# Kernel tuning notes

Measured on AMD Instinct MI355X. Metric: run time of the kernel, lower is better.

The kernel has to match this reference:

```python
import jax, jax.numpy as jnp
import numpy as np

N, D, H, O, E, K = 16384, 512, 512, 64, 8, 2


def _layernorm(x, g, b, eps=1e-5):
    mu = jnp.mean(x, axis=-1, keepdims=True)
    var = jnp.var(x, axis=-1, keepdims=True)
    return (x - mu) * jax.lax.rsqrt(var + eps) * g + b


def _gelu(x):
    return jax.nn.gelu(x, approximate=False)  # torch nn.GELU default (erf)


def setup_inputs() -> dict:
    key = jax.random.key(0)
    ks = jax.random.split(key, 20)
    s = 0.02
    return {
        "x": jax.random.normal(ks[0], (N, D), jnp.float32),
        # gate: Linear(D,H) -> LN(H) -> GELU -> Linear(H,E)
        "g_w1": jax.random.normal(ks[1], (D, H), jnp.float32) * s,
        "g_b1": jnp.zeros((H,), jnp.float32),
        "g_ln_g": jnp.ones((H,), jnp.float32),
        "g_ln_b": jnp.zeros((H,), jnp.float32),
        "g_w2": jax.random.normal(ks[2], (H, E), jnp.float32) * s,
        "g_b2": jnp.zeros((E,), jnp.float32),
        # experts (stacked over E): Linear(D,H)+LN+GELU, Linear(H,H)+LN+GELU, Linear(H,O)
        "e_w1": jax.random.normal(ks[3], (E, D, H), jnp.float32) * s,
        "e_b1": jnp.zeros((E, H), jnp.float32),
        "e_ln1_g": jnp.ones((E, H), jnp.float32),
        "e_ln1_b": jnp.zeros((E, H), jnp.float32),
        "e_w2": jax.random.normal(ks[4], (E, H, H), jnp.float32) * s,
        "e_b2": jnp.zeros((E, H), jnp.float32),
        "e_ln2_g": jnp.ones((E, H), jnp.float32),
        "e_ln2_b": jnp.zeros((E, H), jnp.float32),
        "e_w3": jax.random.normal(ks[5], (E, H, O), jnp.float32) * s,
        "e_b3": jnp.zeros((E, O), jnp.float32),
        # output projection Linear(O,O)
        "p_w": jax.random.normal(ks[6], (O, O), jnp.float32) * s,
        "p_b": jnp.zeros((O,), jnp.float32),
    }


def reference(x, g_w1, g_b1, g_ln_g, g_ln_b, g_w2, g_b2,
              e_w1, e_b1, e_ln1_g, e_ln1_b, e_w2, e_b2, e_ln2_g, e_ln2_b,
              e_w3, e_b3, p_w, p_b):
    n = x.shape[0]
    # --- gate ---
    gh = _gelu(_layernorm(x @ g_w1 + g_b1, g_ln_g, g_ln_b))
    gate_logits = gh @ g_w2 + g_b2                      # [N, E]
    gate_weights = jax.nn.softmax(gate_logits, axis=-1)
    top_k_weights, top_k_indices = jax.lax.top_k(gate_weights, K)
    top_k_weights = top_k_weights / jnp.sum(top_k_weights, axis=-1, keepdims=True)
    # dense per-token expert weights [N, E] (sum of top-k weights routed to each expert)
    w_dense = jnp.zeros((n, e_w1.shape[0]), x.dtype).at[
        jnp.arange(n)[:, None], top_k_indices].add(top_k_weights)
    # --- all experts on all tokens (faithful to dense loop) ---
    h1 = _gelu(_layernorm(jnp.einsum('nd,edh->enh', x, e_w1) + e_b1[:, None, :],
                          e_ln1_g[:, None, :], e_ln1_b[:, None, :]))
    h2 = _gelu(_layernorm(jnp.einsum('enh,ehk->enk', h1, e_w2) + e_b2[:, None, :],
                          e_ln2_g[:, None, :], e_ln2_b[:, None, :]))
    expert_out = jnp.einsum('enh,eho->eno', h2, e_w3) + e_b3[:, None, :]  # [E, N, O]
    combined = jnp.einsum('ne,eno->no', w_dense, expert_out)              # [N, O]
    output = combined @ p_w + p_b
    expert_usage = jnp.mean(gate_weights, axis=0)
    return (output, gate_weights, top_k_indices, top_k_weights, expert_usage)
```

## Files before the change

kernel.cpp:

```cpp
#include <hip/hip_runtime.h>
#include <hip/hip_bf16.h>

#define N_TOK 16384
#define MAX_SLOTS 34080
#define MAX_BLOCKS 216

typedef __attribute__((ext_vector_type(8))) short bf16x8;
typedef __attribute__((ext_vector_type(4))) float f32x4;
typedef unsigned short u16;

__device__ __forceinline__ u16 f2bf(float f) {
  __hip_bfloat16 h = __float2bfloat16(f);
  union { __hip_bfloat16 b; u16 u; } c; c.b = h; return c.u;
}
__device__ __forceinline__ float bfbits2f(u16 u) {
  return __uint_as_float(((unsigned)u) << 16);
}
__device__ __forceinline__ float gelu_erf(float x) {
  return 0.5f * x * (1.0f + erff(x * 0.70710678118654752f));
}
__device__ __forceinline__ float gelu_fast(float x) {
  float u = x * (0.79788456f + 0.035677408f * x * x);
  float ex;
  asm("v_exp_f32 %0, %1" : "=v"(ex) : "v"(-2.8853901f * u));
  float den = 1.0f + ex;
  float r;
  asm("v_rcp_f32 %0, %1" : "=v"(r) : "v"(den));
  return x * r;
}
__device__ __forceinline__ void gload16(const u16* g, char* lds) {
  __builtin_amdgcn_global_load_lds(
      (const __attribute__((address_space(1))) void*)g,
      (__attribute__((address_space(3))) void*)lds, 16, 0, 0);
}

__global__ __launch_bounds__(256) void prep_x(const float* __restrict__ x,
                                              u16* __restrict__ xbf,
                                              u16* __restrict__ xlo) {
  size_t i = (size_t)blockIdx.x * 256 + threadIdx.x;
  float4 v = ((const float4*)x)[i];
  float a[4] = {v.x, v.y, v.z, v.w};
  union { u16 us[4]; unsigned long long ll; } hb, lb;
#pragma unroll
  for (int j = 0; j < 4; ++j) {
    u16 hu = f2bf(a[j]);
    hb.us[j] = hu;
    lb.us[j] = f2bf(a[j] - bfbits2f(hu));
  }
  *(unsigned long long*)(xbf + i * 4) = hb.ll;
  *(unsigned long long*)(xlo + i * 4) = lb.ll;
}

template <int C>
__global__ __launch_bounds__(256) void pack_w(const float* __restrict__ src,
                                              u16* __restrict__ dst, int R) {
  __shared__ float tl[64][65];
  const int e = blockIdx.z;
  const int k0 = blockIdx.x * 64, n0 = blockIdx.y * 64;
  const float* s = src + (size_t)e * R * C;
  const int tr = threadIdx.x >> 2;
  const int tc4 = (threadIdx.x & 3) * 16;
#pragma unroll
  for (int j = 0; j < 4; ++j) {
    float4 v = *(const float4*)(s + (size_t)(k0 + tr) * C + n0 + tc4 + j * 4);
    tl[tr][tc4 + j * 4 + 0] = v.x;
    tl[tr][tc4 + j * 4 + 1] = v.y;
    tl[tr][tc4 + j * 4 + 2] = v.z;
    tl[tr][tc4 + j * 4 + 3] = v.w;
  }
  __syncthreads();
  const int nl = threadIdx.x >> 2;
  const int kl = (threadIdx.x & 3) * 16;
  const int n = n0 + nl;
  const int sx = (n >> 1) & 3;
  const int t = (k0 + kl) >> 5;
  const int q0 = ((k0 + kl) & 31) >> 3;
#pragma unroll
  for (int c = 0; c < 2; ++c) {
    int q = q0 + c;
    int p = q ^ sx;
    union { u16 us[8]; unsigned long long ll[2]; } o;
#pragma unroll
    for (int j = 0; j < 8; ++j) o.us[j] = f2bf(tl[kl + c * 8 + j][nl]);
    u16* d = dst + (((size_t)e * (R / 32) + t) * C + n) * 32 + p * 8;
    ((unsigned long long*)d)[0] = o.ll[0];
    ((unsigned long long*)d)[1] = o.ll[1];
  }
}

__global__ __launch_bounds__(256) void prep_wcat(const float* __restrict__ gw1,
                                                 u16* __restrict__ wp) {
  int idx = blockIdx.x * 256 + threadIdx.x;
  int p = idx & 3;
  int n = (idx >> 2) & 511;
  int t = idx >> 11;
  int q = p ^ ((n >> 1) & 3);
  int k0 = t * 32 + q * 8;
  union { u16 us[8]; unsigned long long ll[2]; } o;
#pragma unroll
  for (int j = 0; j < 8; ++j) {
    int k = k0 + j;
    u16 v;
    if (k < 512) {
      v = f2bf(gw1[k * 512 + n]);
    } else if (k < 1024) {
      float w = gw1[(k - 512) * 512 + n];
      v = f2bf(w - bfbits2f(f2bf(w)));
    } else {
      v = f2bf(gw1[(k - 1024) * 512 + n]);
    }
    o.us[j] = v;
  }
  unsigned long long* d = (unsigned long long*)(wp + (size_t)idx * 8);
  d[0] = o.ll[0];
  d[1] = o.ll[1];
}

__global__ __launch_bounds__(256) void prep_w2t(const float* __restrict__ gw2,
                                                float* __restrict__ w2t) {
  int i = blockIdx.x * 256 + threadIdx.x;
  int e = i >> 9, k = i & 511;
  w2t[i] = gw2[k * 8 + e];
}

template <int FM, int ROUTED, int GATHER, int LNOUT, int FAST>
__global__ __launch_bounds__(512, 2) void gemm_core(
    const u16* __restrict__ A, const u16* __restrict__ A2,
    const u16* __restrict__ Wp, long w_estride, int klen, long osplit,
    const float* __restrict__ bias, int b_estride,
    const float* __restrict__ lng, const float* __restrict__ lnb,
    u16* __restrict__ outb, float* __restrict__ outf,
    const int* __restrict__ slot_token, const int* __restrict__ blk_e,
    const int* __restrict__ blk_tok0) {
  constexpr int BM = FM * 32;
  constexpr int AG = FM * 2;
  constexpr int ABYTES = BM * 64;
  constexpr int BUF = ABYTES + 32768;
  constexpr int NL = AG + 32;
  constexpr int L = (NL + 7) / 8;
  constexpr int TSU = 16384;
  extern __shared__ char smem[];

  const int tid = threadIdx.x;
  const int lane = tid & 63;
  const int wv = tid >> 6;
  const int wm = (wv & 1) * (FM * 16);
  const int wn = (wv >> 1) * 128;
  const int l15 = lane & 15;
  const int lk = lane >> 4;
  const int swzk16 = (lk ^ ((l15 >> 1) & 3)) << 4;

  int e, row0, kt0, kbase;
  if (ROUTED) {
    e = blk_e[blockIdx.x];
    if (e < 0) return;
    row0 = blk_tok0[blockIdx.x];
    kt0 = 0; kbase = 0;
  } else {
    e = 0;
    row0 = blockIdx.x * BM;
    kbase = blockIdx.y * klen;
    kt0 = kbase >> 5;
  }
  const u16* We = Wp + (size_t)e * w_estride;

  const int lrq = lane >> 2;
  const int cse = (((lane & 3) ^ ((lane >> 3) & 3)) << 3);
  size_t off[L];
  int ldsoff[L], typ[L];
#pragma unroll
  for (int i = 0; i < L; ++i) {
    int id = wv + 8 * i;
    if (id >= NL) { typ[i] = 2; off[i] = 0; ldsoff[i] = 0; continue; }
    if (id < AG) {
      int lr = id * 16 + lrq;
      long grow = GATHER ? (long)slot_token[row0 + lr] : (long)(row0 + lr);
      off[i] = (size_t)grow * 512 + cse;
      ldsoff[i] = id * 1024 + lane * 16;
      typ[i] = 0;
    } else {
      int bg = id - AG;
      off[i] = (size_t)bg * 512 + lane * 8;
      ldsoff[i] = ABYTES + bg * 1024 + lane * 16;
      typ[i] = 1;
    }
  }

  auto STAGE = [&](int t, char* b) {
    const int kg = kbase + t * 32;
    const u16* Aseg = A;
    int kc = kg;
    if (A2) {
      if (kg >= 1024) { Aseg = A2; kc = kg - 1024; }
      else if (kg >= 512) kc = kg - 512;
    }
    const u16* Bt = We + (size_t)(kt0 + t) * TSU;
#pragma unroll
    for (int i = 0; i < L; ++i) {
      if (typ[i] == 0)      gload16(Aseg + off[i] + kc, b + ldsoff[i]);
      else if (typ[i] == 1) gload16(Bt + off[i], b + ldsoff[i]);
    }
  };

  f32x4 acc[FM][8];
#pragma unroll
  for (int i = 0; i < FM; ++i)
#pragma unroll
    for (int j = 0; j < 8; ++j) acc[i][j] = (f32x4){0.f, 0.f, 0.f, 0.f};

  const int nt = klen / 32;
  char* buf0 = smem;
  char* buf1 = smem + BUF;

  STAGE(0, buf0);
  __syncthreads();
  for (int t = 0; t < nt; ++t) {
    char* cur = (t & 1) ? buf1 : buf0;
    char* nxt = (t & 1) ? buf0 : buf1;
    if (t + 1 < nt) STAGE(t + 1, nxt);
    char* cB = cur + ABYTES;
    bf16x8 af[FM];
#pragma unroll
    for (int fm = 0; fm < FM; ++fm)
      af[fm] = *(const bf16x8*)(cur + (wm + fm * 16 + l15) * 64 + swzk16);
#pragma unroll
    for (int fn = 0; fn < 8; ++fn) {
      bf16x8 bv = *(const bf16x8*)(cB + (wn + fn * 16 + l15) * 64 + swzk16);
#pragma unroll
      for (int fm = 0; fm < FM; ++fm)
        acc[fm][fn] = __builtin_amdgcn_mfma_f32_16x16x32_bf16(
            af[fm], bv, acc[fm][fn], 0, 0, 0);
    }
    __syncthreads();
  }

  if constexpr (LNOUT) {
    const float* be = bias + (size_t)e * b_estride;
    const float* ge = lng + (size_t)e * b_estride;
    const float* bbe = lnb + (size_t)e * b_estride;
    float bias_v[8], g_v[8], b_v[8];
#pragma unroll
    for (int fn = 0; fn < 8; ++fn) {
      int col = wn + fn * 16 + l15;
      bias_v[fn] = be[col]; g_v[fn] = ge[col]; b_v[fn] = bbe[col];
    }
#pragma unroll
    for (int fm = 0; fm < FM; ++fm)
#pragma unroll
      for (int fn = 0; fn < 8; ++fn)
#pragma unroll
        for (int r = 0; r < 4; ++r) acc[fm][fn][r] += bias_v[fn];

    float* redS1 = (float*)smem;
    float* redS2 = redS1 + 4 * BM;
    const int g = wv >> 1;
#pragma unroll
    for (int fm = 0; fm < FM; ++fm)
#pragma unroll
      for (int r = 0; r < 4; ++r) {
        float a1 = 0.f, a2 = 0.f;
#pragma unroll
        for (int fn = 0; fn < 8; ++fn) {
          float v = acc[fm][fn][r];
          a1 += v; a2 += v * v;
        }
#pragma unroll
        for (int m = 1; m < 16; m <<= 1) {
          a1 += __shfl_xor(a1, m, 64);
          a2 += __shfl_xor(a2, m, 64);
        }
        if (l15 == 0) {
          int row = wm + fm * 16 + lk * 4 + r;
          redS1[g * BM + row] = a1;
          redS2[g * BM + row] = a2;
        }
      }
    __syncthreads();
#pragma unroll
    for (int fm = 0; fm < FM; ++fm)
#pragma unroll
      for (int r = 0; r < 4; ++r) {
        int row = wm + fm * 16 + lk * 4 + r;
        float S1 = 0.f, S2 = 0.f;
#pragma unroll
        for (int q = 0; q < 4; ++q) {
          S1 += redS1[q * BM + row];
          S2 += redS2[q * BM + row];
        }
        float mu = S1 * (1.0f / 512.0f);
        float var = S2 * (1.0f / 512.0f) - mu * mu;
        float rs = rsqrtf(var + 1e-5f);
        size_t rowg = (size_t)(row0 + row);
#pragma unroll
        for (int fn = 0; fn < 8; ++fn) {
          int col = wn + fn * 16 + l15;
          float v = (acc[fm][fn][r] - mu) * rs * g_v[fn] + b_v[fn];
          v = FAST ? gelu_fast(v) : gelu_erf(v);
          outb[rowg * 512 + col] = f2bf(v);
        }
      }
  } else {
    float* dst = outf + (size_t)blockIdx.y * osplit;
#pragma unroll
    for (int fm = 0; fm < FM; ++fm)
#pragma unroll
      for (int r = 0; r < 4; ++r) {
        size_t rowg = (size_t)(row0 + wm + fm * 16 + lk * 4 + r);
#pragma unroll
        for (int fn = 0; fn < 8; ++fn)
          dst[rowg * 512 + wn + fn * 16 + l15] = acc[fm][fn][r];
      }
  }
}

__global__ __launch_bounds__(256) void gate2_topk(
    const float* __restrict__ gh0, const float* __restrict__ gh1,
    const float* __restrict__ b1, const float* __restrict__ lng,
    const float* __restrict__ lnb, const float* __restrict__ w2t,
    const float* __restrict__ b2, float* __restrict__ gwout,
    float* __restrict__ idxout, float* __restrict__ tkwout) {
  const int lane = threadIdx.x & 63;
  const int wv = threadIdx.x >> 6;
  const int t = blockIdx.x * 4 + wv;
  const int c0 = lane * 8;
  float v[8];
  {
    float4 a0 = *(const float4*)(gh0 + (size_t)t * 512 + c0);
    float4 a1 = *(const float4*)(gh0 + (size_t)t * 512 + c0 + 4);
    float4 h0 = *(const float4*)(gh1 + (size_t)t * 512 + c0);
    float4 h1 = *(const float4*)(gh1 + (size_t)t * 512 + c0 + 4);
    float4 bb0 = *(const float4*)(b1 + c0);
    float4 bb1 = *(const float4*)(b1 + c0 + 4);
    v[0] = a0.x + h0.x + bb0.x; v[1] = a0.y + h0.y + bb0.y;
    v[2] = a0.z + h0.z + bb0.z; v[3] = a0.w + h0.w + bb0.w;
    v[4] = a1.x + h1.x + bb1.x; v[5] = a1.y + h1.y + bb1.y;
    v[6] = a1.z + h1.z + bb1.z; v[7] = a1.w + h1.w + bb1.w;
  }
  float s1 = 0.f, s2 = 0.f;
#pragma unroll
  for (int j = 0; j < 8; ++j) { s1 += v[j]; s2 += v[j] * v[j]; }
#pragma unroll
  for (int m = 1; m < 64; m <<= 1) {
    s1 += __shfl_xor(s1, m, 64);
    s2 += __shfl_xor(s2, m, 64);
  }
  float mu = s1 * (1.0f / 512.0f);
  float var = s2 * (1.0f / 512.0f) - mu * mu;
  float rs = rsqrtf(var + 1e-5f);
  float y[8];
  {
    float4 g0 = *(const float4*)(lng + c0);
    float4 g1 = *(const float4*)(lng + c0 + 4);
    float4 q0 = *(const float4*)(lnb + c0);
    float4 q1 = *(const float4*)(lnb + c0 + 4);
    float gg[8] = {g0.x, g0.y, g0.z, g0.w, g1.x, g1.y, g1.z, g1.w};
    float qq[8] = {q0.x, q0.y, q0.z, q0.w, q1.x, q1.y, q1.z, q1.w};
#pragma unroll
    for (int j = 0; j < 8; ++j)
      y[j] = gelu_erf((v[j] - mu) * rs * gg[j] + qq[j]);
  }
  float logit[8];
#pragma unroll
  for (int e = 0; e < 8; ++e) {
    const float4* wr = (const float4*)(w2t + e * 512 + c0);
    float4 w0 = wr[0], w1 = wr[1];
    float p = y[0] * w0.x + y[1] * w0.y + y[2] * w0.z + y[3] * w0.w +
              y[4] * w1.x + y[5] * w1.y + y[6] * w1.z + y[7] * w1.w;
#pragma unroll
    for (int m = 1; m < 64; m <<= 1) p += __shfl_xor(p, m, 64);
    logit[e] = p + b2[e];
  }
  if (lane == 0) {
    float mx = logit[0];
#pragma unroll
    for (int e = 1; e < 8; ++e) mx = fmaxf(mx, logit[e]);
    float w[8], ssum = 0.f;
#pragma unroll
    for (int e = 0; e < 8; ++e) { w[e] = expf(logit[e] - mx); ssum += w[e]; }
    float inv = 1.0f / ssum;
#pragma unroll
    for (int e = 0; e < 8; ++e) w[e] *= inv;
    float w1v = -1.f, w2v = -1.f; int i1 = 0, i2 = 0;
#pragma unroll
    for (int e = 0; e < 8; ++e) {
      float vv = w[e];
      if (vv > w1v)      { w2v = w1v; i2 = i1; w1v = vv; i1 = e; }
      else if (vv > w2v) { w2v = vv; i2 = e; }
    }
    float s = w1v + w2v;
#pragma unroll
    for (int e = 0; e < 8; ++e) gwout[t * 8 + e] = w[e];
    idxout[t * 2] = (float)i1; idxout[t * 2 + 1] = (float)i2;
    tkwout[t * 2] = w1v / s;   tkwout[t * 2 + 1] = w2v / s;
  }
}

__global__ __launch_bounds__(256) void usage_k(const float* __restrict__ gw,
                                               float* __restrict__ usage) {
  __shared__ float r[256];
  int e = blockIdx.x;
  float s = 0.f;
  for (int t = threadIdx.x; t < N_TOK; t += 256) s += gw[t * 8 + e];
  r[threadIdx.x] = s;
  __syncthreads();
  for (int st = 128; st > 0; st >>= 1) {
    if (threadIdx.x < st) r[threadIdx.x] += r[threadIdx.x + st];
    __syncthreads();
  }
  if (threadIdx.x == 0) usage[e] = r[0] * (1.0f / (float)N_TOK);
}

__global__ __launch_bounds__(256) void count_hist(const float* __restrict__ idxout,
                                                  int* __restrict__ blk_cnt) {
  __shared__ int h[8];
  if (threadIdx.x < 8) h[threadIdx.x] = 0;
  __syncthreads();
  int t = blockIdx.x * 256 + threadIdx.x;
  int e0 = (int)idxout[t * 2], e1 = (int)idxout[t * 2 + 1];
  atomicAdd(&h[e0], 1);
  atomicAdd(&h[e1], 1);
  __syncthreads();
  if (threadIdx.x < 8) blk_cnt[blockIdx.x * 8 + threadIdx.x] = h[threadIdx.x];
}

__global__ __launch_bounds__(512) void k_offsets2(
    const int* __restrict__ blk_cnt, int* __restrict__ sbase,
    int* __restrict__ blk_e, int* __restrict__ blk_tok0) {
  __shared__ int cnt[64][8];
  __shared__ int ecnt[8];
  __shared__ int offs[8];
  __shared__ int nbtot;
  const int tid = threadIdx.x;
  cnt[tid >> 3][tid & 7] = blk_cnt[tid];
  __syncthreads();
  if (tid < 8) {
    int s = 0;
    for (int b = 0; b < 64; ++b) s += cnt[b][tid];
    ecnt[tid] = s;
  }
  __syncthreads();
  if (tid == 0) {
    int off = 0, nb = 0;
    for (int e = 0; e < 8; ++e) {
      offs[e] = off;
      int nbe = (ecnt[e] + 159) / 160;
      off += nbe * 160;
      nb += nbe;
    }
    nbtot = nb;
  }
  __syncthreads();
  {
    int b = tid >> 3, e = tid & 7;
    int s = offs[e];
    for (int bp = 0; bp < b; ++bp) s += cnt[bp][e];
    sbase[tid] = s;
  }
  const int q = (nbtot + 7) >> 3;
  for (int b = tid; b < MAX_BLOCKS; b += 512) {
    int xcd = b & 7, i = b >> 3;
    int j = xcd * q + i;
    int be = -1, bt = 0;
    if (i < q && j < nbtot) {
      int acc = 0;
#pragma unroll
      for (int e = 0; e < 8; ++e) {
        int nbe = (ecnt[e] + 159) / 160;
        if (j >= acc && j < acc + nbe) { be = e; bt = offs[e] + (j - acc) * 160; }
        acc += nbe;
      }
    }
    blk_e[b] = be;
    blk_tok0[b] = bt;
  }
}

__global__ __launch_bounds__(256) void k_padinit(int* __restrict__ slot_token,
                                                 float* __restrict__ slot_w) {
  int i = blockIdx.x * 256 + threadIdx.x;
  if (i < MAX_SLOTS) { slot_token[i] = 0; slot_w[i] = 0.f; }
}

__global__ __launch_bounds__(256) void k_scatter2(
    const float* __restrict__ idxout, const float* __restrict__ tkwout,
    const int* __restrict__ sbase, int* __restrict__ slot_token,
    float* __restrict__ slot_w, int* __restrict__ tok_slot) {
  __shared__ int lpos[8];
  if (threadIdx.x < 8) lpos[threadIdx.x] = 0;
  __syncthreads();
  int t = blockIdx.x * 256 + threadIdx.x;
#pragma unroll
  for (int k = 0; k < 2; ++k) {
    int e = (int)idxout[t * 2 + k];
    int lr = atomicAdd(&lpos[e], 1);
    int s = sbase[blockIdx.x * 8 + e] + lr;
    slot_token[s] = t;
    slot_w[s] = tkwout[t * 2 + k];
    tok_slot[t * 2 + k] = s;
  }
}

__global__ __launch_bounds__(512) void gemm3_eo(
    const u16* __restrict__ h, const u16* __restrict__ w3p,
    const float* __restrict__ b3, const float* __restrict__ slot_w,
    const int* __restrict__ blk_e, const int* __restrict__ blk_tok0,
    float* __restrict__ eo) {
  constexpr int ABYTES = 10240;
  constexpr int BUF = ABYTES + 4096;
  __shared__ char smem[2][BUF];
  int e = blk_e[blockIdx.x];
  if (e < 0) return;
  int row0 = blk_tok0[blockIdx.x];

  const int tid = threadIdx.x;
  const int lane = tid & 63;
  const int wv = tid >> 6;
  const int wm = (wv & 1) * 80;
  const int wn = (wv >> 1) * 16;
  const int l15 = lane & 15, lk = lane >> 4;
  const int swzk16 = (lk ^ ((l15 >> 1) & 3)) << 4;
  const u16* we = w3p + (size_t)e * 32768;

  const int lrq = lane >> 2;
  const int cse = (((lane & 3) ^ ((lane >> 3) & 3)) << 3);
  size_t off[2];
  int ldsoff[2], typ[2];
#pragma unroll
  for (int i = 0; i < 2; ++i) {
    int id = wv + 8 * i;
    if (id >= 14) { typ[i] = 2; off[i] = 0; ldsoff[i] = 0; continue; }
    if (id < 10) {
      off[i] = (size_t)(row0 + id * 16 + lrq) * 512 + cse;
      ldsoff[i] = id * 1024 + lane * 16;
      typ[i] = 0;
    } else {
      int bg = id - 10;
      off[i] = (size_t)bg * 512 + lane * 8;
      ldsoff[i] = ABYTES + bg * 1024 + lane * 16;
      typ[i] = 1;
    }
  }

  auto STAGE = [&](int t, char* b) {
#pragma unroll
    for (int i = 0; i < 2; ++i) {
      if (typ[i] == 0)      gload16(h + off[i] + t * 32, b + ldsoff[i]);
      else if (typ[i] == 1) gload16(we + (size_t)t * 2048 + off[i], b + ldsoff[i]);
    }
  };

  f32x4 acc[5];
#pragma unroll
  for (int j = 0; j < 5; ++j) acc[j] = (f32x4){0.f, 0.f, 0.f, 0.f};

  STAGE(0, smem[0]);
  __syncthreads();
  for (int t = 0; t < 16; ++t) {
    char* cur = smem[t & 1];
    if (t + 1 < 16) STAGE(t + 1, smem[(t + 1) & 1]);
    char* cB = cur + ABYTES;
    bf16x8 bv = *(const bf16x8*)(cB + (wn + l15) * 64 + swzk16);
#pragma unroll
    for (int fm = 0; fm < 5; ++fm) {
      bf16x8 a = *(const bf16x8*)(cur + (wm + fm * 16 + l15) * 64 + swzk16);
      acc[fm] = __builtin_amdgcn_mfma_f32_16x16x32_bf16(a, bv, acc[fm], 0, 0, 0);
    }
    __syncthreads();
  }

#pragma unroll
  for (int fm = 0; fm < 5; ++fm)
#pragma unroll
    for (int r = 0; r < 4; ++r) {
      int row = wm + fm * 16 + lk * 4 + r;
      float w = slot_w[row0 + row];
      int col = wn + l15;
      eo[(size_t)(row0 + row) * 64 + col] = w * (acc[fm][r] + b3[e * 64 + col]);
    }
}

__global__ __launch_bounds__(256) void combine_proj(
    const float* __restrict__ eo, const int* __restrict__ tok_slot,
    const float* __restrict__ pw, const float* __restrict__ pb,
    float* __restrict__ outp) {
  __shared__ float cs[64][68];
  __shared__ float pws[64][68];
  const int t0 = blockIdx.x * 64;
  const int tq = threadIdx.x & 3;
  const int tt = threadIdx.x >> 2;
#pragma unroll
  for (int j = 0; j < 4; ++j) {
    float4 v = *(const float4*)(pw + tt * 64 + tq * 16 + j * 4);
    *(float4*)&pws[tt][tq * 16 + j * 4] = v;
  }
  {
    int t = t0 + tt;
    int s1 = tok_slot[t * 2], s2 = tok_slot[t * 2 + 1];
#pragma unroll
    for (int j = 0; j < 4; ++j) {
      float4 a = *(const float4*)(eo + (size_t)s1 * 64 + tq * 16 + j * 4);
      float4 b = *(const float4*)(eo + (size_t)s2 * 64 + tq * 16 + j * 4);
      float4 c = {a.x + b.x, a.y + b.y, a.z + b.z, a.w + b.w};
      *(float4*)&cs[tt][tq * 16 + j * 4] = c;
    }
  }
  __syncthreads();
  float o[16];
#pragma unroll
  for (int i = 0; i < 16; ++i) o[i] = 0.f;
  for (int j = 0; j < 64; ++j) {
    float c = cs[tt][j];
#pragma unroll
    for (int q4 = 0; q4 < 4; ++q4) {
      float4 p = *(const float4*)&pws[j][tq * 16 + q4 * 4];
      o[q4 * 4 + 0] += c * p.x;
      o[q4 * 4 + 1] += c * p.y;
      o[q4 * 4 + 2] += c * p.z;
      o[q4 * 4 + 3] += c * p.w;
    }
  }
#pragma unroll
  for (int i = 0; i < 16; ++i)
    outp[(size_t)(t0 + tt) * 64 + tq * 16 + i] = o[i] + pb[tq * 16 + i];
}

extern "C" void kernel_launch(void* const* d_in, const int* in_sizes, int n_in,
                              void* d_out, int out_size, void* d_ws, size_t ws_size,
                              hipStream_t stream) {
  const float* x      = (const float*)d_in[0];
  const float* g_w1   = (const float*)d_in[1];
  const float* g_b1   = (const float*)d_in[2];
  const float* g_lng  = (const float*)d_in[3];
  const float* g_lnb  = (const float*)d_in[4];
  const float* g_w2   = (const float*)d_in[5];
  const float* g_b2   = (const float*)d_in[6];
  const float* e_w1   = (const float*)d_in[7];
  const float* e_b1   = (const float*)d_in[8];
  const float* e_ln1g = (const float*)d_in[9];
  const float* e_ln1b = (const float*)d_in[10];
  const float* e_w2   = (const float*)d_in[11];
  const float* e_b2   = (const float*)d_in[12];
  const float* e_ln2g = (const float*)d_in[13];
  const float* e_ln2b = (const float*)d_in[14];
  const float* e_w3   = (const float*)d_in[15];
  const float* e_b3   = (const float*)d_in[16];
  const float* p_w    = (const float*)d_in[17];
  const float* p_b    = (const float*)d_in[18];

  char* ws = (char*)d_ws;
  u16*   x_bf  = (u16*)(ws);
  u16*   x_lo  = (u16*)(ws + (16ull << 20));
  u16*   e_w1p = (u16*)(ws + (32ull << 20));
  u16*   e_w2p = (u16*)(ws + (36ull << 20));
  u16*   e_w3p = (u16*)(ws + (40ull << 20));
  u16*   wcat  = (u16*)(ws + (41ull << 20));
  float* w2t   = (float*)(ws + (43ull << 20));
  float* gh0   = (float*)(ws + (44ull << 20));
  float* gh1   = (float*)(ws + (76ull << 20));
  u16*   h     = (u16*)(ws + (44ull << 20));
  float* eo    = (float*)(ws + (112ull << 20));
  int*   slot_token = (int*)(ws + (121ull << 20));
  float* slot_w     = (float*)(ws + (121ull << 20) + (1ull << 18));
  int*   tok_slot   = (int*)(ws + (121ull << 20) + (2ull << 18));
  int*   blk_cnt    = (int*)(ws + (122ull << 20));
  int*   sbase      = blk_cnt + 512;
  int*   blk_e      = blk_cnt + 1024;
  int*   blk_tok0   = blk_cnt + 2048;
  if (ws_size < (123ull << 20)) return;

  float* fout = (float*)d_out;
  float* o_output = fout;
  float* o_gatew  = fout + 1048576;
  float* o_idx    = fout + 1179648;
  float* o_topw   = fout + 1212416;
  float* o_usage  = fout + 1245184;

  (void)hipFuncSetAttribute((const void*)gemm_core<4, 0, 0, 0, 0>,
                            hipFuncAttributeMaxDynamicSharedMemorySize, 81920);
  (void)hipFuncSetAttribute((const void*)gemm_core<5, 1, 1, 1, 1>,
                            hipFuncAttributeMaxDynamicSharedMemorySize, 86016);
  (void)hipFuncSetAttribute((const void*)gemm_core<5, 1, 0, 1, 1>,
                            hipFuncAttributeMaxDynamicSharedMemorySize, 86016);

  prep_x<<<8192, 256, 0, stream>>>(x, x_bf, x_lo);
  pack_w<512><<<dim3(8, 8, 8), 256, 0, stream>>>(e_w1, e_w1p, 512);
  pack_w<512><<<dim3(8, 8, 8), 256, 0, stream>>>(e_w2, e_w2p, 512);
  pack_w<64><<<dim3(8, 1, 8), 256, 0, stream>>>(e_w3, e_w3p, 512);
  prep_wcat<<<384, 256, 0, stream>>>(g_w1, wcat);
  prep_w2t<<<16, 256, 0, stream>>>(g_w2, w2t);

  gemm_core<4, 0, 0, 0, 0><<<dim3(N_TOK / 128, 2), 512, 81920, stream>>>(
      x_bf, x_lo, wcat, 0, 768, (long)N_TOK * 512, nullptr, 0,
      nullptr, nullptr, nullptr, gh0, nullptr, nullptr, nullptr);
  gate2_topk<<<N_TOK / 4, 256, 0, stream>>>(gh0, gh1, g_b1, g_lng, g_lnb,
                                            w2t, g_b2, o_gatew, o_idx, o_topw);
  usage_k<<<8, 256, 0, stream>>>(o_gatew, o_usage);

  count_hist<<<64, 256, 0, stream>>>(o_idx, blk_cnt);
  k_offsets2<<<1, 512, 0, stream>>>(blk_cnt, sbase, blk_e, blk_tok0);
  k_padinit<<<(MAX_SLOTS + 255) / 256, 256, 0, stream>>>(slot_token, slot_w);
  k_scatter2<<<64, 256, 0, stream>>>(o_idx, o_topw, sbase, slot_token, slot_w,
                                     tok_slot);

  gemm_core<5, 1, 1, 1, 1><<<MAX_BLOCKS, 512, 86016, stream>>>(
      x_bf, nullptr, e_w1p, 512 * 512, 512, 0, e_b1, 512,
      e_ln1g, e_ln1b, h, nullptr, slot_token, blk_e, blk_tok0);
  gemm_core<5, 1, 0, 1, 1><<<MAX_BLOCKS, 512, 86016, stream>>>(
      h, nullptr, e_w2p, 512 * 512, 512, 0, e_b2, 512,
      e_ln2g, e_ln2b, h, nullptr, slot_token, blk_e, blk_tok0);
  gemm3_eo<<<MAX_BLOCKS, 512, 0, stream>>>(h, e_w3p, e_b3, slot_w, blk_e,
                                           blk_tok0, eo);
  combine_proj<<<N_TOK / 64, 256, 0, stream>>>(eo, tok_slot, p_w, p_b, o_output);
}
```

Baseline: 206.8 us.

## Fuse expert layer-2 GEMM with LN/GELU and layer-3 projection

Replaces the separate layer-2 expert GEMM (which wrote h back to global memory) and the gemm3_eo kernel with one kernel. After the layer-2 GEMM, LayerNorm and GELU are applied in registers. The activations are then staged through LDS in chunks and multiplied by W3 to produce the weighted expert outputs directly. This removes one kernel launch and the global write and re-read of the 160x512 bf16 intermediate per block. In exchange it adds register pressure and a serialized chunk loop with extra barriers in the epilogue.

After: 236.5 us. 14.4% more time.

```diff
diff --git a/kernel.cpp b/kernel.cpp
--- a/kernel.cpp
+++ b/kernel.cpp
@@ -311,6 +311,224 @@
           dst[rowg * 512 + wn + fn * 16 + l15] = acc[fm][fn][r];
       }
   }
+}
+
+__global__ __launch_bounds__(512, 2) void gemm_l2eo(
+    const u16* __restrict__ A, const u16* __restrict__ Wp,
+    const u16* __restrict__ W3p, const float* __restrict__ bias,
+    const float* __restrict__ lng, const float* __restrict__ lnb,
+    const float* __restrict__ b3, const float* __restrict__ slot_w,
+    const int* __restrict__ blk_e, const int* __restrict__ blk_tok0,
+    float* __restrict__ eo) {
+  constexpr int FM = 5, BM = 160, AG = 10;
+  constexpr int ABYTES = BM * 64;
+  constexpr int BUF = ABYTES + 32768;
+  constexpr int NL = AG + 32;
+  constexpr int L = 6;
+  constexpr int TSU = 16384;
+  extern __shared__ char smem[];
+
+  const int tid = threadIdx.x;
+  const int lane = tid & 63;
+  const int wv = tid >> 6;
+  const int wm = (wv & 1) * 80;
+  const int wn = (wv >> 1) * 128;
+  const int l15 = lane & 15;
+  const int lk = lane >> 4;
+  const int swzk16 = (lk ^ ((l15 >> 1) & 3)) << 4;
+
+  int e = blk_e[blockIdx.x];
+  if (e < 0) return;
+  const int row0 = blk_tok0[blockIdx.x];
+  const u16* We = Wp + (size_t)e * (512 * 512);
+
+  const int lrq = lane >> 2;
+  const int cse = (((lane & 3) ^ ((lane >> 3) & 3)) << 3);
+  size_t off[L];
+  int ldsoff[L], typ[L];
+#pragma unroll
+  for (int i = 0; i < L; ++i) {
+    int id = wv + 8 * i;
+    if (id >= NL) { typ[i] = 2; off[i] = 0; ldsoff[i] = 0; continue; }
+    if (id < AG) {
+      off[i] = (size_t)(row0 + id * 16 + lrq) * 512 + cse;
+      ldsoff[i] = id * 1024 + lane * 16;
+      typ[i] = 0;
+    } else {
+      int bg = id - AG;
+      off[i] = (size_t)bg * 512 + lane * 8;
+      ldsoff[i] = ABYTES + bg * 1024 + lane * 16;
+      typ[i] = 1;
+    }
+  }
+
+  auto STAGE = [&](int t, char* b) {
+    const u16* Bt = We + (size_t)t * TSU;
+#pragma unroll
+    for (int i = 0; i < L; ++i) {
+      if (typ[i] == 0)      gload16(A + off[i] + t * 32, b + ldsoff[i]);
+      else if (typ[i] == 1) gload16(Bt + off[i], b + ldsoff[i]);
+    }
+  };
+
+  f32x4 acc[FM][8];
+#pragma unroll
+  for (int i = 0; i < FM; ++i)
+#pragma unroll
+    for (int j = 0; j < 8; ++j) acc[i][j] = (f32x4){0.f, 0.f, 0.f, 0.f};
+
+  char* buf0 = smem;
+  char* buf1 = smem + BUF;
+
+  STAGE(0, buf0);
+  __syncthreads();
+  for (int t = 0; t < 16; ++t) {
+    char* cur = (t & 1) ? buf1 : buf0;
+    char* nxt = (t & 1) ? buf0 : buf1;
+    if (t + 1 < 16) STAGE(t + 1, nxt);
+    char* cB = cur + ABYTES;
+    bf16x8 af[FM];
+#pragma unroll
+    for (int fm = 0; fm < FM; ++fm)
+      af[fm] = *(const bf16x8*)(cur + (wm + fm * 16 + l15) * 64 + swzk16);
+#pragma unroll
+    for (int fn = 0; fn < 8; ++fn) {
+      bf16x8 bv = *(const bf16x8*)(cB + (wn + fn * 16 + l15) * 64 + swzk16);
+#pragma unroll
+      for (int fm = 0; fm < FM; ++fm)
+        acc[fm][fn] = __builtin_amdgcn_mfma_f32_16x16x32_bf16(
+            af[fm], bv, acc[fm][fn], 0, 0, 0);
+    }
+    __syncthreads();
+  }
+
+  {
+    const float* be = bias + (size_t)e * 512;
+    const float* ge = lng + (size_t)e * 512;
+    const float* bbe = lnb + (size_t)e * 512;
+    float bias_v[8], g_v[8], b_v[8];
+#pragma unroll
+    for (int fn = 0; fn < 8; ++fn) {
+      int col = wn + fn * 16 + l15;
+      bias_v[fn] = be[col]; g_v[fn] = ge[col]; b_v[fn] = bbe[col];
+    }
+#pragma unroll
+    for (int fm = 0; fm < FM; ++fm)
+#pragma unroll
+      for (int fn = 0; fn < 8; ++fn)
+#pragma unroll
+        for (int r = 0; r < 4; ++r) acc[fm][fn][r] += bias_v[fn];
+
+    float* redS1 = (float*)smem;
+    float* redS2 = redS1 + 4 * BM;
+    const int g = wv >> 1;
+#pragma unroll
+    for (int fm = 0; fm < FM; ++fm)
+#pragma unroll
+      for (int r = 0; r < 4; ++r) {
+        float a1 = 0.f, a2 = 0.f;
+#pragma unroll
+        for (int fn = 0; fn < 8; ++fn) {
+          float v = acc[fm][fn][r];
+          a1 += v; a2 += v * v;
+        }
+#pragma unroll
+        for (int m = 1; m < 16; m <<= 1) {
+          a1 += __shfl_xor(a1, m, 64);
+          a2 += __shfl_xor(a2, m, 64);
+        }
+        if (l15 == 0) {
+          int row = wm + fm * 16 + lk * 4 + r;
+          redS1[g * BM + row] = a1;
+          redS2[g * BM + row] = a2;
+        }
+      }
+    __syncthreads();
+#pragma unroll
+    for (int fm = 0; fm < FM; ++fm)
+#pragma unroll
+      for (int r = 0; r < 4; ++r) {
+        int row = wm + fm * 16 + lk * 4 + r;
+        float S1 = 0.f, S2 = 0.f;
+#pragma unroll
+        for (int q = 0; q < 4; ++q) {
+          S1 += redS1[q * BM + row];
+          S2 += redS2[q * BM + row];
+        }
+        float mu = S1 * (1.0f / 512.0f);
+        float var = S2 * (1.0f / 512.0f) - mu * mu;
+        float rs = rsqrtf(var + 1e-5f);
+#pragma unroll
+        for (int fn = 0; fn < 8; ++fn) {
+          float v = (acc[fm][fn][r] - mu) * rs * g_v[fn] + b_v[fn];
+          acc[fm][fn][r] = gelu_fast(v);
+        }
+      }
+  }
+
+  const u16* W3e = W3p + (size_t)e * 32768;
+  char* A2 = smem;
+  char* B3 = smem + 20480;
+  const int g2 = wv >> 1;
+  const int wn3 = g2 * 16;
+  float b3v = b3[e * 64 + wn3 + l15];
+  float swr[5][4];
+#pragma unroll
+  for (int fm = 0; fm < 5; ++fm)
+#pragma unroll
+    for (int r = 0; r < 4; ++r)
+      swr[fm][r] = slot_w[row0 + wm + fm * 16 + lk * 4 + r];
+
+  f32x4 eacc[5];
+#pragma unroll
+  for (int j = 0; j < 5; ++j) eacc[j] = (f32x4){0.f, 0.f, 0.f, 0.f};
+
+#pragma unroll
+  for (int cc = 0; cc < 8; ++cc) {
+    __syncthreads();
+    if ((cc >> 1) == g2) {
+      constexpr int FNB = 0;
+#pragma unroll
+      for (int fd = 0; fd < 4; ++fd) {
+        const int fn = (cc & 1) * 4 + fd;
+#pragma unroll
+        for (int fm = 0; fm < 5; ++fm)
+#pragma unroll
+          for (int r = 0; r < 4; ++r) {
+            int row = wm + fm * 16 + lk * 4 + r;
+            int colb = (fd * 16 + l15) * 2;
+            int p = (colb >> 4) ^ (row & 7);
+            *(u16*)(A2 + row * 128 + p * 16 + (colb & 15)) =
+                f2bf(acc[fm][fn][r]);
+          }
+      }
+      (void)FNB;
+    }
+    gload16(W3e + (size_t)(2 * cc) * 2048 + (size_t)tid * 8,
+            B3 + (size_t)tid * 16);
+    __syncthreads();
+#pragma unroll
+    for (int ss = 0; ss < 2; ++ss) {
+      bf16x8 bv = *(const bf16x8*)(B3 + ss * 4096 + (wn3 + l15) * 64 + swzk16);
+#pragma unroll
+      for (int fm = 0; fm < 5; ++fm) {
+        int row = wm + fm * 16 + l15;
+        int p = (ss * 4 + lk) ^ (row & 7);
+        bf16x8 av = *(const bf16x8*)(A2 + row * 128 + p * 16);
+        eacc[fm] = __builtin_amdgcn_mfma_f32_16x16x32_bf16(av, bv, eacc[fm],
+                                                           0, 0, 0);
+      }
+    }
+  }
+
+#pragma unroll
+  for (int fm = 0; fm < 5; ++fm)
+#pragma unroll
+    for (int r = 0; r < 4; ++r) {
+      int row = wm + fm * 16 + lk * 4 + r;
+      eo[(size_t)(row0 + row) * 64 + wn3 + l15] =
+          swr[fm][r] * (eacc[fm][r] + b3v);
+    }
 }
 
 __global__ __launch_bounds__(256) void gate2_topk(
@@ -500,85 +718,6 @@
   }
 }
 
-__global__ __launch_bounds__(512) void gemm3_eo(
-    const u16* __restrict__ h, const u16* __restrict__ w3p,
-    const float* __restrict__ b3, const float* __restrict__ slot_w,
-    const int* __restrict__ blk_e, const int* __restrict__ blk_tok0,
-    float* __restrict__ eo) {
-  constexpr int ABYTES = 10240;
-  constexpr int BUF = ABYTES + 4096;
-  __shared__ char smem[2][BUF];
-  int e = blk_e[blockIdx.x];
-  if (e < 0) return;
-  int row0 = blk_tok0[blockIdx.x];
-
-  const int tid = threadIdx.x;
-  const int lane = tid & 63;
-  const int wv = tid >> 6;
-  const int wm = (wv & 1) * 80;
-  const int wn = (wv >> 1) * 16;
-  const int l15 = lane & 15, lk = lane >> 4;
-  const int swzk16 = (lk ^ ((l15 >> 1) & 3)) << 4;
-  const u16* we = w3p + (size_t)e * 32768;
-
-  const int lrq = lane >> 2;
-  const int cse = (((lane & 3) ^ ((lane >> 3) & 3)) << 3);
-  size_t off[2];
-  int ldsoff[2], typ[2];
-#pragma unroll
-  for (int i = 0; i < 2; ++i) {
-    int id = wv + 8 * i;
-    if (id >= 14) { typ[i] = 2; off[i] = 0; ldsoff[i] = 0; continue; }
-    if (id < 10) {
-      off[i] = (size_t)(row0 + id * 16 + lrq) * 512 + cse;
-      ldsoff[i] = id * 1024 + lane * 16;
-      typ[i] = 0;
-    } else {
-      int bg = id - 10;
-      off[i] = (size_t)bg * 512 + lane * 8;
-      ldsoff[i] = ABYTES + bg * 1024 + lane * 16;
-      typ[i] = 1;
-    }
-  }
-
-  auto STAGE = [&](int t, char* b) {
-#pragma unroll
-    for (int i = 0; i < 2; ++i) {
-      if (typ[i] == 0)      gload16(h + off[i] + t * 32, b + ldsoff[i]);
-      else if (typ[i] == 1) gload16(we + (size_t)t * 2048 + off[i], b + ldsoff[i]);
-    }
-  };
-
-  f32x4 acc[5];
-#pragma unroll
-  for (int j = 0; j < 5; ++j) acc[j] = (f32x4){0.f, 0.f, 0.f, 0.f};
-
-  STAGE(0, smem[0]);
-  __syncthreads();
-  for (int t = 0; t < 16; ++t) {
-    char* cur = smem[t & 1];
-    if (t + 1 < 16) STAGE(t + 1, smem[(t + 1) & 1]);
-    char* cB = cur + ABYTES;
-    bf16x8 bv = *(const bf16x8*)(cB + (wn + l15) * 64 + swzk16);
-#pragma unroll
-    for (int fm = 0; fm < 5; ++fm) {
-      bf16x8 a = *(const bf16x8*)(cur + (wm + fm * 16 + l15) * 64 + swzk16);
-      acc[fm] = __builtin_amdgcn_mfma_f32_16x16x32_bf16(a, bv, acc[fm], 0, 0, 0);
-    }
-    __syncthreads();
-  }
-
-#pragma unroll
-  for (int fm = 0; fm < 5; ++fm)
-#pragma unroll
-    for (int r = 0; r < 4; ++r) {
-      int row = wm + fm * 16 + lk * 4 + r;
-      float w = slot_w[row0 + row];
-      int col = wn + l15;
-      eo[(size_t)(row0 + row) * 64 + col] = w * (acc[fm][r] + b3[e * 64 + col]);
-    }
-}
-
 __global__ __launch_bounds__(256) void combine_proj(
     const float* __restrict__ eo, const int* __restrict__ tok_slot,
     const float* __restrict__ pw, const float* __restrict__ pb,
@@ -679,7 +818,7 @@
                             hipFuncAttributeMaxDynamicSharedMemorySize, 81920);
   (void)hipFuncSetAttribute((const void*)gemm_core<5, 1, 1, 1, 1>,
                             hipFuncAttributeMaxDynamicSharedMemorySize, 86016);
-  (void)hipFuncSetAttribute((const void*)gemm_core<5, 1, 0, 1, 1>,
+  (void)hipFuncSetAttribute((const void*)gemm_l2eo,
                             hipFuncAttributeMaxDynamicSharedMemorySize, 86016);
 
   prep_x<<<8192, 256, 0, stream>>>(x, x_bf, x_lo);
@@ -705,10 +844,8 @@
   gemm_core<5, 1, 1, 1, 1><<<MAX_BLOCKS, 512, 86016, stream>>>(
       x_bf, nullptr, e_w1p, 512 * 512, 512, 0, e_b1, 512,
       e_ln1g, e_ln1b, h, nullptr, slot_token, blk_e, blk_tok0);
-  gemm_core<5, 1, 0, 1, 1><<<MAX_BLOCKS, 512, 86016, stream>>>(
-      h, nullptr, e_w2p, 512 * 512, 512, 0, e_b2, 512,
-      e_ln2g, e_ln2b, h, nullptr, slot_token, blk_e, blk_tok0);
-  gemm3_eo<<<MAX_BLOCKS, 512, 0, stream>>>(h, e_w3p, e_b3, slot_w, blk_e,
-                                           blk_tok0, eo);
+  gemm_l2eo<<<MAX_BLOCKS, 512, 86016, stream>>>(
+      h, e_w2p, e_w3p, e_b2, e_ln2g, e_ln2b, e_b3, slot_w,
+      blk_e, blk_tok0, eo);
   combine_proj<<<N_TOK / 64, 256, 0, stream>>>(eo, tok_slot, p_w, p_b, o_output);
 }
```
